# Performance work log

Measured on AMD Instinct MI355X. Metric: run time of the kernel, lower is better.

## Reference

```python
import jax, jax.numpy as jnp
import numpy as np

N, NOBJ, M, H, W = 512, 16, 8192, 128, 128


def _rand_rotations(key, n):
    A = jax.random.normal(key, (n, 3, 3), dtype=jnp.float32)
    q, r = jnp.linalg.qr(A)
    q = q * jnp.sign(jnp.diagonal(r, axis1=-2, axis2=-1))[:, None, :]
    det = jnp.linalg.det(q)  # +-1; flip first column if det == -1
    q = q.at[:, :, 0].multiply(det[:, None])
    return q


def setup_inputs() -> dict:
    key = jax.random.key(0)
    ks = jax.random.split(key, 10)
    obj_id = jax.random.randint(ks[0], (N,), 0, NOBJ, dtype=jnp.int32)
    # realistic pinhole intrinsics (pixels), slight per-sample jitter
    base_K = jnp.array([[600.0, 0.0, 64.0], [0.0, 600.0, 64.0], [0.0, 0.0, 1.0]], jnp.float32)
    cam_K = base_K[None] + jax.random.normal(ks[1], (N, 3, 3)) * jnp.array(
        [[5.0, 0.0, 1.0], [0.0, 5.0, 1.0], [0.0, 0.0, 0.0]], jnp.float32)
    gt_R = _rand_rotations(ks[2], N)
    # small rotational perturbation for pred
    pred_R = _rand_rotations(ks[3], N) @ gt_R
    gt_t = jnp.concatenate([jax.random.normal(ks[4], (N, 2)) * 20.0,
                            500.0 + jax.random.uniform(ks[4], (N, 1)) * 300.0], axis=-1)
    pred_t = gt_t + jax.random.normal(ks[5], (N, 3)) * 5.0
    mesh_points = jax.random.normal(ks[6], (NOBJ, M, 3)) * 50.0  # mm-scale meshes
    diameters = 150.0 + jax.random.uniform(ks[7], (NOBJ,)) * 150.0
    gt_coord_3d_roi = jax.random.normal(ks[8], (N, 3, H, W)) * 50.0
    gt_mask_vis_roi = jax.random.bernoulli(ks[9], 0.4, (N, 1, H, W))
    return dict(obj_id=obj_id, cam_K=cam_K, gt_cam_R_m2c=gt_R, gt_cam_t_m2c=gt_t,
                pred_cam_R_m2c=pred_R, pred_cam_t_m2c=pred_t,
                gt_coord_3d_roi=gt_coord_3d_roi, gt_mask_vis_roi=gt_mask_vis_roi,
                mesh_points=mesh_points, diameters=diameters)


def _project(K, x):
    # K: [N,3,3], x: [N,...,3] -> pixel coords [N,...,2]
    h = jnp.einsum('nij,n...j->n...i', K, x)
    return h[..., :2] / h[..., 2:3]


def reference(obj_id, cam_K, gt_cam_R_m2c, gt_cam_t_m2c, pred_cam_R_m2c,
              pred_cam_t_m2c, gt_coord_3d_roi, gt_mask_vis_roi, mesh_points, diameters):
    # RE (degrees)
    R_diff = pred_cam_R_m2c @ jnp.swapaxes(gt_cam_R_m2c, -2, -1)
    trace = R_diff[..., 0, 0] + R_diff[..., 1, 1] + R_diff[..., 2, 2]
    re = jnp.arccos((jnp.clip(trace, -1.0, 3.0) - 1.0) * 0.5) * (180.0 / jnp.pi)
    # TE (cm)
    te = jnp.linalg.norm(pred_cam_t_m2c - gt_cam_t_m2c, axis=-1) * 100.0
    # ADD: mean distance between transformed mesh points, / diameter
    pts = mesh_points[obj_id]                      # [N,M,3]
    dR = pred_cam_R_m2c - gt_cam_R_m2c
    dt = pred_cam_t_m2c - gt_cam_t_m2c
    diff = jnp.einsum('nij,nmj->nmi', dR, pts) + dt[:, None, :]
    ad = jnp.linalg.norm(diff, axis=-1).mean(axis=-1) / diameters[obj_id]
    # PROJ: mean projected distance over mesh points
    xp = jnp.einsum('nij,nmj->nmi', pred_cam_R_m2c, pts) + pred_cam_t_m2c[:, None, :]
    xg = jnp.einsum('nij,nmj->nmi', gt_cam_R_m2c, pts) + gt_cam_t_m2c[:, None, :]
    pj = jnp.linalg.norm(_project(cam_K, xp) - _project(cam_K, xg), axis=-1).mean(axis=-1)
    # PROJ-visible: same over visible ROI pixels (masked mean instead of ragged gather)
    verts = jnp.transpose(gt_coord_3d_roi, (0, 2, 3, 1))  # [N,H,W,3]
    vp = jnp.einsum('nij,nhwj->nhwi', pred_cam_R_m2c, verts) + pred_cam_t_m2c[:, None, None, :]
    vg = jnp.einsum('nij,nhwj->nhwi', gt_cam_R_m2c, verts) + gt_cam_t_m2c[:, None, None, :]
    d = jnp.linalg.norm(_project(cam_K, vp) - _project(cam_K, vg), axis=-1)  # [N,H,W]
    mask = gt_mask_vis_roi[:, 0].astype(d.dtype)
    pv = (d * mask).sum(axis=(1, 2)) / jnp.maximum(mask.sum(axis=(1, 2)), 1.0)
    return re, te, ad, pj, pv
```

## Files before the change

kernel.cpp:

```cpp
#include <hip/hip_runtime.h>
#include <math.h>

#define NS    512
#define NOBJ  16
#define MPTS  8192
#define HH    128
#define WW    128
#define HW    (HH * WW)
#define BLOCK 256
#define SPLIT 4
#define NWAVE (BLOCK / 64)
#define P_IT  (HW / 4 / SPLIT / BLOCK)
#define M_IT  (MPTS / SPLIT / (BLOCK * 4))

__device__ __forceinline__ float frcp(float x)  { return __builtin_amdgcn_rcpf(x); }
__device__ __forceinline__ float fsqrt(float x) { return __builtin_amdgcn_sqrtf(x); }
__device__ __forceinline__ float rfl(float x) {
    return __int_as_float(__builtin_amdgcn_readfirstlane(__float_as_int(x)));
}
__device__ __forceinline__ void sched_fence() {
#if __has_builtin(__builtin_amdgcn_sched_barrier)
    __builtin_amdgcn_sched_barrier(0);
#endif
}

__device__ __forceinline__ void fuse_proj(const float* __restrict__ cam_K,
                                          const float* __restrict__ R,
                                          const float* __restrict__ t, int n,
                                          float A[9], float b[3]) {
    float K[9], Rr[9], tt[3];
#pragma unroll
    for (int i = 0; i < 9; ++i) { K[i] = cam_K[n * 9 + i]; Rr[i] = R[n * 9 + i]; }
#pragma unroll
    for (int i = 0; i < 3; ++i) tt[i] = t[n * 3 + i];
#pragma unroll
    for (int r = 0; r < 3; ++r) {
#pragma unroll
        for (int c = 0; c < 3; ++c)
            A[r * 3 + c] = rfl(K[r * 3 + 0] * Rr[0 * 3 + c]
                             + K[r * 3 + 1] * Rr[1 * 3 + c]
                             + K[r * 3 + 2] * Rr[2 * 3 + c]);
        b[r] = rfl(K[r * 3 + 0] * tt[0] + K[r * 3 + 1] * tt[1] + K[r * 3 + 2] * tt[2]);
    }
}

__global__ __attribute__((amdgpu_flat_work_group_size(BLOCK, BLOCK),
                          amdgpu_waves_per_eu(3, 4)))
void score_partial(
    const int*   __restrict__ obj_id,
    const float* __restrict__ cam_K,
    const float* __restrict__ gt_R,
    const float* __restrict__ gt_t,
    const float* __restrict__ pr_R,
    const float* __restrict__ pr_t,
    const float* __restrict__ coord,
    const int*   __restrict__ mask,
    const float* __restrict__ mesh,
    float*       __restrict__ ws)
{
    const int b   = blockIdx.x;
    const int n   = b >> 2;
    const int c   = b & (SPLIT - 1);
    const int tid = threadIdx.x;

    float Ap[9], Ag[9], bp[3], bg[3], dR[9], dt[3];
    fuse_proj(cam_K, pr_R, pr_t, n, Ap, bp);
    fuse_proj(cam_K, gt_R, gt_t, n, Ag, bg);
#pragma unroll
    for (int i = 0; i < 9; ++i) dR[i] = rfl(pr_R[n * 9 + i] - gt_R[n * 9 + i]);
#pragma unroll
    for (int i = 0; i < 3; ++i) dt[i] = rfl(pr_t[n * 3 + i] - gt_t[n * 3 + i]);
    const int obj = __builtin_amdgcn_readfirstlane(obj_id[n]);

    const float* cx = coord + (size_t)n * 3 * HW;
    const float4* cx4 = (const float4*)cx;
    const float4* cy4 = (const float4*)(cx + HW);
    const float4* cz4 = (const float4*)(cx + 2 * HW);
    const int4*   mk4 = (const int4*)(mask + (size_t)n * HW);
    const float4* mp4 = (const float4*)(mesh + (size_t)obj * MPTS * 3);

    float4 AX[P_IT], AY[P_IT], AZ[P_IT];
    int4   AM[P_IT];
#pragma unroll
    for (int it = 0; it < P_IT; ++it) {
        const int p = c * (HW / 4 / SPLIT) + it * BLOCK + tid;
        AX[it] = cx4[p];
        AY[it] = cy4[p];
        AZ[it] = cz4[p];
        AM[it] = mk4[p];
    }
    float4 MF[M_IT][3];
#pragma unroll
    for (int it = 0; it < M_IT; ++it) {
        const int k = c * (MPTS / SPLIT / 4) + it * BLOCK + tid;
        MF[it][0] = mp4[k * 3 + 0];
        MF[it][1] = mp4[k * 3 + 1];
        MF[it][2] = mp4[k * 3 + 2];
    }

    sched_fence();

    float s_pv = 0.0f, s_m = 0.0f;
#pragma unroll
    for (int it = 0; it < P_IT; ++it) {
        const float xs[4] = {AX[it].x, AX[it].y, AX[it].z, AX[it].w};
        const float ys[4] = {AY[it].x, AY[it].y, AY[it].z, AY[it].w};
        const float zs[4] = {AZ[it].x, AZ[it].y, AZ[it].z, AZ[it].w};
        const int   ms[4] = {AM[it].x, AM[it].y, AM[it].z, AM[it].w};
#pragma unroll
        for (int j = 0; j < 4; ++j) {
            const float x = xs[j], y = ys[j], z = zs[j];
            const float hpx = fmaf(Ap[0], x, fmaf(Ap[1], y, fmaf(Ap[2], z, bp[0])));
            const float hpy = fmaf(Ap[3], x, fmaf(Ap[4], y, fmaf(Ap[5], z, bp[1])));
            const float hpz = fmaf(Ap[6], x, fmaf(Ap[7], y, fmaf(Ap[8], z, bp[2])));
            const float hgx = fmaf(Ag[0], x, fmaf(Ag[1], y, fmaf(Ag[2], z, bg[0])));
            const float hgy = fmaf(Ag[3], x, fmaf(Ag[4], y, fmaf(Ag[5], z, bg[1])));
            const float hgz = fmaf(Ag[6], x, fmaf(Ag[7], y, fmaf(Ag[8], z, bg[2])));
            const float iwp = frcp(hpz), iwg = frcp(hgz);
            const float du = fmaf(hpx, iwp, -hgx * iwg);
            const float dv = fmaf(hpy, iwp, -hgy * iwg);
            const float d  = fsqrt(fmaf(du, du, dv * dv));
            const float fm = (ms[j] != 0) ? 1.0f : 0.0f;
            s_pv += d * fm;
            s_m  += fm;
        }
    }

    float s_ad = 0.0f, s_pj = 0.0f;
#pragma unroll
    for (int it = 0; it < M_IT; ++it) {
        const float4 f0 = MF[it][0], f1 = MF[it][1], f2 = MF[it][2];
        const float px[4] = {f0.x, f0.w, f1.z, f2.y};
        const float py[4] = {f0.y, f1.x, f1.w, f2.z};
        const float pz[4] = {f0.z, f1.y, f2.x, f2.w};
#pragma unroll
        for (int j = 0; j < 4; ++j) {
            const float x = px[j], y = py[j], z = pz[j];
            const float dx = fmaf(dR[0], x, fmaf(dR[1], y, fmaf(dR[2], z, dt[0])));
            const float dy = fmaf(dR[3], x, fmaf(dR[4], y, fmaf(dR[5], z, dt[1])));
            const float dz = fmaf(dR[6], x, fmaf(dR[7], y, fmaf(dR[8], z, dt[2])));
            s_ad += fsqrt(fmaf(dx, dx, fmaf(dy, dy, dz * dz)));
            const float hpx = fmaf(Ap[0], x, fmaf(Ap[1], y, fmaf(Ap[2], z, bp[0])));
            const float hpy = fmaf(Ap[3], x, fmaf(Ap[4], y, fmaf(Ap[5], z, bp[1])));
            const float hpz = fmaf(Ap[6], x, fmaf(Ap[7], y, fmaf(Ap[8], z, bp[2])));
            const float hgx = fmaf(Ag[0], x, fmaf(Ag[1], y, fmaf(Ag[2], z, bg[0])));
            const float hgy = fmaf(Ag[3], x, fmaf(Ag[4], y, fmaf(Ag[5], z, bg[1])));
            const float hgz = fmaf(Ag[6], x, fmaf(Ag[7], y, fmaf(Ag[8], z, bg[2])));
            const float iwp = frcp(hpz), iwg = frcp(hgz);
            const float du = fmaf(hpx, iwp, -hgx * iwg);
            const float dv = fmaf(hpy, iwp, -hgy * iwg);
            s_pj += fsqrt(fmaf(du, du, dv * dv));
        }
    }

    float vals[4] = {s_ad, s_pj, s_pv, s_m};
#pragma unroll
    for (int k = 0; k < 4; ++k)
#pragma unroll
        for (int off = 32; off > 0; off >>= 1)
            vals[k] += __shfl_down(vals[k], off, 64);

    __shared__ float red[4][NWAVE];
    const int wave = tid >> 6, lane = tid & 63;
    if (lane == 0) {
#pragma unroll
        for (int k = 0; k < 4; ++k) red[k][wave] = vals[k];
    }
    __syncthreads();
    if (tid == 0) {
#pragma unroll
        for (int k = 0; k < 4; ++k) {
            float s = 0.0f;
#pragma unroll
            for (int w = 0; w < NWAVE; ++w) s += red[k][w];
            ws[(size_t)(n * SPLIT + c) * 4 + k] = s;
        }
    }
}

__global__ __launch_bounds__(256) void score_reduce(
    const float* __restrict__ ws,
    const int*   __restrict__ obj_id,
    const float* __restrict__ gt_R,
    const float* __restrict__ gt_t,
    const float* __restrict__ pr_R,
    const float* __restrict__ pr_t,
    const float* __restrict__ diam,
    float*       __restrict__ out)
{
    const int n = blockIdx.x * blockDim.x + threadIdx.x;
    if (n >= NS) return;

    float ad = 0.0f, pj = 0.0f, pv = 0.0f, m = 0.0f;
#pragma unroll
    for (int cb = 0; cb < SPLIT; ++cb) {
        const float* p = ws + (size_t)(n * SPLIT + cb) * 4;
        ad += p[0]; pj += p[1]; pv += p[2]; m += p[3];
    }

    float trace = 0.0f;
#pragma unroll
    for (int i = 0; i < 9; ++i) trace += pr_R[n * 9 + i] * gt_R[n * 9 + i];
    trace = fminf(fmaxf(trace, -1.0f), 3.0f);
    const float dx = pr_t[n * 3 + 0] - gt_t[n * 3 + 0];
    const float dy = pr_t[n * 3 + 1] - gt_t[n * 3 + 1];
    const float dz = pr_t[n * 3 + 2] - gt_t[n * 3 + 2];

    const float dia = diam[obj_id[n]];
    out[0 * NS + n] = acosf((trace - 1.0f) * 0.5f) * (180.0f / 3.14159265358979323846f);
    out[1 * NS + n] = sqrtf(dx * dx + dy * dy + dz * dz) * 100.0f;
    out[2 * NS + n] = ad * (1.0f / MPTS) / dia;
    out[3 * NS + n] = pj * (1.0f / MPTS);
    out[4 * NS + n] = pv / fmaxf(m, 1.0f);
}

extern "C" void kernel_launch(void* const* d_in, const int* in_sizes, int n_in,
                              void* d_out, int out_size, void* d_ws, size_t ws_size,
                              hipStream_t stream) {
    const int*   obj_id = (const int*)  d_in[0];
    const float* cam_K  = (const float*)d_in[1];
    const float* gt_R   = (const float*)d_in[2];
    const float* gt_t   = (const float*)d_in[3];
    const float* pr_R   = (const float*)d_in[4];
    const float* pr_t   = (const float*)d_in[5];
    const float* coord  = (const float*)d_in[6];
    const int*   mask   = (const int*)  d_in[7];
    const float* mesh   = (const float*)d_in[8];
    const float* diam   = (const float*)d_in[9];
    float* out = (float*)d_out;
    float* ws  = (float*)d_ws;

    score_partial<<<NS * SPLIT, BLOCK, 0, stream>>>(obj_id, cam_K, gt_R, gt_t, pr_R,
                                                    pr_t, coord, mask, mesh, ws);
    score_reduce<<<(NS + 255) / 256, 256, 0, stream>>>(ws, obj_id, gt_R, gt_t,
                                                       pr_R, pr_t, diam, out);
}
```

Baseline: 192.0 us.

## Fuse partial and reduce kernels into one block-per-sample kernel with prefetch pipeline

Replaces the two-kernel scheme (4 blocks per sample writing partials, then a reduce kernel) with one 512-thread block per sample that writes final outputs directly. ROI data is streamed through a 4-slot register ring with 3-deep software prefetch and nontemporal loads, instead of loading everything up front. Mesh loads are moved after the ROI loop. This removes a launch and the workspace round-trip, at the cost of fewer blocks (512) to fill the GPU and a serialised per-block pipeline.

```diff
diff --git a/kernel.cpp b/kernel.cpp
--- a/kernel.cpp
+++ b/kernel.cpp
@@ -7,11 +7,13 @@
 #define HH    128
 #define WW    128
 #define HW    (HH * WW)
-#define BLOCK 256
-#define SPLIT 4
+#define BLOCK 512
 #define NWAVE (BLOCK / 64)
-#define P_IT  (HW / 4 / SPLIT / BLOCK)
-#define M_IT  (MPTS / SPLIT / (BLOCK * 4))
+#define P_IT  (HW / 4 / BLOCK)
+#define M_IT  (MPTS / 4 / BLOCK)
+
+typedef float f4 __attribute__((ext_vector_type(4)));
+typedef int   i4 __attribute__((ext_vector_type(4)));
 
 __device__ __forceinline__ float frcp(float x)  { return __builtin_amdgcn_rcpf(x); }
 __device__ __forceinline__ float fsqrt(float x) { return __builtin_amdgcn_sqrtf(x); }
@@ -21,6 +23,20 @@
 __device__ __forceinline__ void sched_fence() {
 #if __has_builtin(__builtin_amdgcn_sched_barrier)
     __builtin_amdgcn_sched_barrier(0);
+#endif
+}
+__device__ __forceinline__ f4 ntl_f4(const f4* p) {
+#if __has_builtin(__builtin_nontemporal_load)
+    return __builtin_nontemporal_load(p);
+#else
+    return *p;
+#endif
+}
+__device__ __forceinline__ i4 ntl_i4(const i4* p) {
+#if __has_builtin(__builtin_nontemporal_load)
+    return __builtin_nontemporal_load(p);
+#else
+    return *p;
 #endif
 }
 
@@ -45,8 +61,8 @@
 }
 
 __global__ __attribute__((amdgpu_flat_work_group_size(BLOCK, BLOCK),
-                          amdgpu_waves_per_eu(3, 4)))
-void score_partial(
+                          amdgpu_waves_per_eu(4, 4)))
+void score_kernel(
     const int*   __restrict__ obj_id,
     const float* __restrict__ cam_K,
     const float* __restrict__ gt_R,
@@ -56,11 +72,10 @@
     const float* __restrict__ coord,
     const int*   __restrict__ mask,
     const float* __restrict__ mesh,
-    float*       __restrict__ ws)
+    const float* __restrict__ diam,
+    float*       __restrict__ out)
 {
-    const int b   = blockIdx.x;
-    const int n   = b >> 2;
-    const int c   = b & (SPLIT - 1);
+    const int n   = blockIdx.x;
     const int tid = threadIdx.x;
 
     float Ap[9], Ag[9], bp[3], bg[3], dR[9], dt[3];
@@ -73,40 +88,40 @@
     const int obj = __builtin_amdgcn_readfirstlane(obj_id[n]);
 
     const float* cx = coord + (size_t)n * 3 * HW;
-    const float4* cx4 = (const float4*)cx;
-    const float4* cy4 = (const float4*)(cx + HW);
-    const float4* cz4 = (const float4*)(cx + 2 * HW);
-    const int4*   mk4 = (const int4*)(mask + (size_t)n * HW);
-    const float4* mp4 = (const float4*)(mesh + (size_t)obj * MPTS * 3);
-
-    float4 AX[P_IT], AY[P_IT], AZ[P_IT];
-    int4   AM[P_IT];
+    const f4* cx4 = (const f4*)cx;
+    const f4* cy4 = (const f4*)(cx + HW);
+    const f4* cz4 = (const f4*)(cx + 2 * HW);
+    const i4* mk4 = (const i4*)(mask + (size_t)n * HW);
+
+    f4 AX[4], AY[4], AZ[4];
+    i4 AM[4];
+#pragma unroll
+    for (int t = 0; t < 3; ++t) {
+        const int p = t * BLOCK + tid;
+        AX[t] = ntl_f4(cx4 + p);
+        AY[t] = ntl_f4(cy4 + p);
+        AZ[t] = ntl_f4(cz4 + p);
+        AM[t] = ntl_i4(mk4 + p);
+    }
+
+    float s_pv = 0.0f, s_m = 0.0f;
 #pragma unroll
     for (int it = 0; it < P_IT; ++it) {
-        const int p = c * (HW / 4 / SPLIT) + it * BLOCK + tid;
-        AX[it] = cx4[p];
-        AY[it] = cy4[p];
-        AZ[it] = cz4[p];
-        AM[it] = mk4[p];
-    }
-    float4 MF[M_IT][3];
-#pragma unroll
-    for (int it = 0; it < M_IT; ++it) {
-        const int k = c * (MPTS / SPLIT / 4) + it * BLOCK + tid;
-        MF[it][0] = mp4[k * 3 + 0];
-        MF[it][1] = mp4[k * 3 + 1];
-        MF[it][2] = mp4[k * 3 + 2];
-    }
-
-    sched_fence();
-
-    float s_pv = 0.0f, s_m = 0.0f;
-#pragma unroll
-    for (int it = 0; it < P_IT; ++it) {
-        const float xs[4] = {AX[it].x, AX[it].y, AX[it].z, AX[it].w};
-        const float ys[4] = {AY[it].x, AY[it].y, AY[it].z, AY[it].w};
-        const float zs[4] = {AZ[it].x, AZ[it].y, AZ[it].z, AZ[it].w};
-        const int   ms[4] = {AM[it].x, AM[it].y, AM[it].z, AM[it].w};
+        if (it + 3 < P_IT) {
+            const int t = it + 3;
+            const int s = t & 3;
+            const int p = t * BLOCK + tid;
+            AX[s] = ntl_f4(cx4 + p);
+            AY[s] = ntl_f4(cy4 + p);
+            AZ[s] = ntl_f4(cz4 + p);
+            AM[s] = ntl_i4(mk4 + p);
+        }
+        sched_fence();
+        const int s = it & 3;
+        const float xs[4] = {AX[s].x, AX[s].y, AX[s].z, AX[s].w};
+        const float ys[4] = {AY[s].x, AY[s].y, AY[s].z, AY[s].w};
+        const float zs[4] = {AZ[s].x, AZ[s].y, AZ[s].z, AZ[s].w};
+        const int   ms[4] = {AM[s].x, AM[s].y, AM[s].z, AM[s].w};
 #pragma unroll
         for (int j = 0; j < 4; ++j) {
             const float x = xs[j], y = ys[j], z = zs[j];
@@ -126,10 +141,21 @@
         }
     }
 
+    const f4* mp4 = (const f4*)(mesh + (size_t)obj * MPTS * 3);
+    f4 MF[M_IT][3];
+#pragma unroll
+    for (int it = 0; it < M_IT; ++it) {
+        const int k = it * BLOCK + tid;
+        MF[it][0] = mp4[k * 3 + 0];
+        MF[it][1] = mp4[k * 3 + 1];
+        MF[it][2] = mp4[k * 3 + 2];
+    }
+    sched_fence();
+
     float s_ad = 0.0f, s_pj = 0.0f;
 #pragma unroll
     for (int it = 0; it < M_IT; ++it) {
-        const float4 f0 = MF[it][0], f1 = MF[it][1], f2 = MF[it][2];
+        const f4 f0 = MF[it][0], f1 = MF[it][1], f2 = MF[it][2];
         const float px[4] = {f0.x, f0.w, f1.z, f2.y};
         const float py[4] = {f0.y, f1.x, f1.w, f2.z};
         const float pz[4] = {f0.z, f1.y, f2.x, f2.w};
@@ -167,51 +193,31 @@
         for (int k = 0; k < 4; ++k) red[k][wave] = vals[k];
     }
     __syncthreads();
+
     if (tid == 0) {
+        float tot[4];
 #pragma unroll
         for (int k = 0; k < 4; ++k) {
             float s = 0.0f;
 #pragma unroll
             for (int w = 0; w < NWAVE; ++w) s += red[k][w];
-            ws[(size_t)(n * SPLIT + c) * 4 + k] = s;
-        }
-    }
-}
-
-__global__ __launch_bounds__(256) void score_reduce(
-    const float* __restrict__ ws,
-    const int*   __restrict__ obj_id,
-    const float* __restrict__ gt_R,
-    const float* __restrict__ gt_t,
-    const float* __restrict__ pr_R,
-    const float* __restrict__ pr_t,
-    const float* __restrict__ diam,
-    float*       __restrict__ out)
-{
-    const int n = blockIdx.x * blockDim.x + threadIdx.x;
-    if (n >= NS) return;
-
-    float ad = 0.0f, pj = 0.0f, pv = 0.0f, m = 0.0f;
-#pragma unroll
-    for (int cb = 0; cb < SPLIT; ++cb) {
-        const float* p = ws + (size_t)(n * SPLIT + cb) * 4;
-        ad += p[0]; pj += p[1]; pv += p[2]; m += p[3];
-    }
-
-    float trace = 0.0f;
-#pragma unroll
-    for (int i = 0; i < 9; ++i) trace += pr_R[n * 9 + i] * gt_R[n * 9 + i];
-    trace = fminf(fmaxf(trace, -1.0f), 3.0f);
-    const float dx = pr_t[n * 3 + 0] - gt_t[n * 3 + 0];
-    const float dy = pr_t[n * 3 + 1] - gt_t[n * 3 + 1];
-    const float dz = pr_t[n * 3 + 2] - gt_t[n * 3 + 2];
-
-    const float dia = diam[obj_id[n]];
-    out[0 * NS + n] = acosf((trace - 1.0f) * 0.5f) * (180.0f / 3.14159265358979323846f);
-    out[1 * NS + n] = sqrtf(dx * dx + dy * dy + dz * dz) * 100.0f;
-    out[2 * NS + n] = ad * (1.0f / MPTS) / dia;
-    out[3 * NS + n] = pj * (1.0f / MPTS);
-    out[4 * NS + n] = pv / fmaxf(m, 1.0f);
+            tot[k] = s;
+        }
+        float Rg9[9], Rp9[9];
+#pragma unroll
+        for (int i = 0; i < 9; ++i) { Rg9[i] = gt_R[n * 9 + i]; Rp9[i] = pr_R[n * 9 + i]; }
+        float trace = 0.0f;
+#pragma unroll
+        for (int i = 0; i < 9; ++i) trace += Rp9[i] * Rg9[i];
+        trace = fminf(fmaxf(trace, -1.0f), 3.0f);
+        const float te = sqrtf(dt[0] * dt[0] + dt[1] * dt[1] + dt[2] * dt[2]) * 100.0f;
+
+        out[0 * NS + n] = acosf((trace - 1.0f) * 0.5f) * (180.0f / 3.14159265358979323846f);
+        out[1 * NS + n] = te;
+        out[2 * NS + n] = tot[0] * (1.0f / MPTS) / diam[obj];
+        out[3 * NS + n] = tot[1] * (1.0f / MPTS);
+        out[4 * NS + n] = tot[2] / fmaxf(tot[3], 1.0f);
+    }
 }
 
 extern "C" void kernel_launch(void* const* d_in, const int* in_sizes, int n_in,
@@ -228,10 +234,7 @@
     const float* mesh   = (const float*)d_in[8];
     const float* diam   = (const float*)d_in[9];
     float* out = (float*)d_out;
-    float* ws  = (float*)d_ws;
-
-    score_partial<<<NS * SPLIT, BLOCK, 0, stream>>>(obj_id, cam_K, gt_R, gt_t, pr_R,
-                                                    pr_t, coord, mask, mesh, ws);
-    score_reduce<<<(NS + 255) / 256, 256, 0, stream>>>(ws, obj_id, gt_R, gt_t,
-                                                       pr_R, pr_t, diam, out);
-}
+
+    score_kernel<<<NS, BLOCK, 0, stream>>>(obj_id, cam_K, gt_R, gt_t, pr_R, pr_t,
+                                           coord, mask, mesh, diam, out);
+}
```

After: 184.4 us. 4.0% less time.

## Stage ROI pixel tiles into LDS via async global_load_lds with staged waits

Applied to the files above, without the earlier changes.

Replaces the per-thread register prefetch of coord and mask float4s with direct global-to-LDS DMA (global_load_lds), issued as four tiles per block. Each tile's compute starts after a partial vmcnt wait, so later tiles keep loading while earlier ones are processed. The aim is to cut VGPR pressure and overlap memory with compute. In exchange each block now holds a 64 KB LDS buffer, which caps blocks per CU. The waves_per_eu hint is also removed, so occupancy may drop.

```diff
diff --git a/kernel.cpp b/kernel.cpp
--- a/kernel.cpp
+++ b/kernel.cpp
@@ -1,17 +1,26 @@
 #include <hip/hip_runtime.h>
 #include <math.h>
 
-#define NS    512
-#define NOBJ  16
-#define MPTS  8192
-#define HH    128
-#define WW    128
-#define HW    (HH * WW)
-#define BLOCK 256
-#define SPLIT 4
-#define NWAVE (BLOCK / 64)
-#define P_IT  (HW / 4 / SPLIT / BLOCK)
-#define M_IT  (MPTS / SPLIT / (BLOCK * 4))
+#define NS     512
+#define NOBJ   16
+#define MPTS   8192
+#define HH     128
+#define WW     128
+#define HW     (HH * WW)
+#define BLOCK  256
+#define NWAVE  (BLOCK / 64)
+#define SPLIT  4
+#define CHUNK  (HW / SPLIT)
+#define TILE   1024
+#define NTILE  (CHUNK / TILE)
+#define SEG    (TILE / NWAVE)
+#define M_IT   (MPTS / SPLIT / (BLOCK * 4))
+
+typedef float f4 __attribute__((ext_vector_type(4)));
+typedef int   i4 __attribute__((ext_vector_type(4)));
+
+typedef const void __attribute__((address_space(1)))* gas1_t;
+typedef void       __attribute__((address_space(3)))* las3_t;
 
 __device__ __forceinline__ float frcp(float x)  { return __builtin_amdgcn_rcpf(x); }
 __device__ __forceinline__ float fsqrt(float x) { return __builtin_amdgcn_sqrtf(x); }
@@ -22,6 +31,11 @@
 #if __has_builtin(__builtin_amdgcn_sched_barrier)
     __builtin_amdgcn_sched_barrier(0);
 #endif
+}
+#define WAIT_VM(n) __builtin_amdgcn_s_waitcnt((n) | (7 << 4) | (0xF << 8))
+
+__device__ __forceinline__ void dma16(const void* g, void* l) {
+    __builtin_amdgcn_global_load_lds((gas1_t)g, (las3_t)l, 16, 0, 0);
 }
 
 __device__ __forceinline__ void fuse_proj(const float* __restrict__ cam_K,
@@ -44,9 +58,50 @@
     }
 }
 
-__global__ __attribute__((amdgpu_flat_work_group_size(BLOCK, BLOCK),
-                          amdgpu_waves_per_eu(3, 4)))
-void score_partial(
+__device__ __forceinline__ void stage_tile(const float* cx, const float* cy,
+                                           const float* cz, const int* mk,
+                                           float* lds, int slot, int gofs, int wofs) {
+    float* base = lds + slot * (4 * TILE) + wofs;
+    dma16(cx + gofs, base + 0 * TILE);
+    dma16(cy + gofs, base + 1 * TILE);
+    dma16(cz + gofs, base + 2 * TILE);
+    dma16((const float*)mk + gofs, base + 3 * TILE);
+}
+
+__device__ __forceinline__ void compute_tile(const float* lds, int slot, int wofs,
+                                             int lane, const float Ap[9],
+                                             const float Ag[9], const float bp[3],
+                                             const float bg[3],
+                                             float& s_pv, float& s_m) {
+    const float* base = lds + slot * (4 * TILE) + wofs + 4 * lane;
+    const f4 vx = *(const f4*)(base + 0 * TILE);
+    const f4 vy = *(const f4*)(base + 1 * TILE);
+    const f4 vz = *(const f4*)(base + 2 * TILE);
+    const i4 mm = *(const i4*)(base + 3 * TILE);
+    const float xs[4] = {vx.x, vx.y, vx.z, vx.w};
+    const float ys[4] = {vy.x, vy.y, vy.z, vy.w};
+    const float zs[4] = {vz.x, vz.y, vz.z, vz.w};
+    const int   ms[4] = {mm.x, mm.y, mm.z, mm.w};
+#pragma unroll
+    for (int j = 0; j < 4; ++j) {
+        const float x = xs[j], y = ys[j], z = zs[j];
+        const float hpx = fmaf(Ap[0], x, fmaf(Ap[1], y, fmaf(Ap[2], z, bp[0])));
+        const float hpy = fmaf(Ap[3], x, fmaf(Ap[4], y, fmaf(Ap[5], z, bp[1])));
+        const float hpz = fmaf(Ap[6], x, fmaf(Ap[7], y, fmaf(Ap[8], z, bp[2])));
+        const float hgx = fmaf(Ag[0], x, fmaf(Ag[1], y, fmaf(Ag[2], z, bg[0])));
+        const float hgy = fmaf(Ag[3], x, fmaf(Ag[4], y, fmaf(Ag[5], z, bg[1])));
+        const float hgz = fmaf(Ag[6], x, fmaf(Ag[7], y, fmaf(Ag[8], z, bg[2])));
+        const float iwp = frcp(hpz), iwg = frcp(hgz);
+        const float du = fmaf(hpx, iwp, -hgx * iwg);
+        const float dv = fmaf(hpy, iwp, -hgy * iwg);
+        const float d  = fsqrt(fmaf(du, du, dv * dv));
+        const float fm = (ms[j] != 0) ? 1.0f : 0.0f;
+        s_pv += d * fm;
+        s_m  += fm;
+    }
+}
+
+__global__ __launch_bounds__(BLOCK) void score_partial(
     const int*   __restrict__ obj_id,
     const float* __restrict__ cam_K,
     const float* __restrict__ gt_R,
@@ -58,10 +113,16 @@
     const float* __restrict__ mesh,
     float*       __restrict__ ws)
 {
-    const int b   = blockIdx.x;
-    const int n   = b >> 2;
-    const int c   = b & (SPLIT - 1);
-    const int tid = threadIdx.x;
+    __shared__ float lds[4 * 4 * TILE];
+    __shared__ float red[4][NWAVE];
+
+    const int b    = blockIdx.x;
+    const int n    = b >> 2;
+    const int c    = b & (SPLIT - 1);
+    const int tid  = threadIdx.x;
+    const int w    = tid >> 6;
+    const int lane = tid & 63;
+    const int wofs = w * SEG;
 
     float Ap[9], Ag[9], bp[3], bg[3], dR[9], dt[3];
     fuse_proj(cam_K, pr_R, pr_t, n, Ap, bp);
@@ -73,23 +134,19 @@
     const int obj = __builtin_amdgcn_readfirstlane(obj_id[n]);
 
     const float* cx = coord + (size_t)n * 3 * HW;
-    const float4* cx4 = (const float4*)cx;
-    const float4* cy4 = (const float4*)(cx + HW);
-    const float4* cz4 = (const float4*)(cx + 2 * HW);
-    const int4*   mk4 = (const int4*)(mask + (size_t)n * HW);
-    const float4* mp4 = (const float4*)(mesh + (size_t)obj * MPTS * 3);
-
-    float4 AX[P_IT], AY[P_IT], AZ[P_IT];
-    int4   AM[P_IT];
-#pragma unroll
-    for (int it = 0; it < P_IT; ++it) {
-        const int p = c * (HW / 4 / SPLIT) + it * BLOCK + tid;
-        AX[it] = cx4[p];
-        AY[it] = cy4[p];
-        AZ[it] = cz4[p];
-        AM[it] = mk4[p];
-    }
-    float4 MF[M_IT][3];
+    const float* cy = cx + HW;
+    const float* cz = cx + 2 * HW;
+    const int*   mk = mask + (size_t)n * HW;
+    const int chunkBase = c * CHUNK;
+    const int laneofs   = wofs + 4 * lane;
+
+    stage_tile(cx, cy, cz, mk, lds, 0, chunkBase + 0 * TILE + laneofs, wofs);
+    stage_tile(cx, cy, cz, mk, lds, 1, chunkBase + 1 * TILE + laneofs, wofs);
+    stage_tile(cx, cy, cz, mk, lds, 2, chunkBase + 2 * TILE + laneofs, wofs);
+    stage_tile(cx, cy, cz, mk, lds, 3, chunkBase + 3 * TILE + laneofs, wofs);
+
+    const f4* mp4 = (const f4*)(mesh + (size_t)obj * MPTS * 3);
+    f4 MF[M_IT][3];
 #pragma unroll
     for (int it = 0; it < M_IT; ++it) {
         const int k = c * (MPTS / SPLIT / 4) + it * BLOCK + tid;
@@ -97,39 +154,22 @@
         MF[it][1] = mp4[k * 3 + 1];
         MF[it][2] = mp4[k * 3 + 2];
     }
-
     sched_fence();
 
     float s_pv = 0.0f, s_m = 0.0f;
-#pragma unroll
-    for (int it = 0; it < P_IT; ++it) {
-        const float xs[4] = {AX[it].x, AX[it].y, AX[it].z, AX[it].w};
-        const float ys[4] = {AY[it].x, AY[it].y, AY[it].z, AY[it].w};
-        const float zs[4] = {AZ[it].x, AZ[it].y, AZ[it].z, AZ[it].w};
-        const int   ms[4] = {AM[it].x, AM[it].y, AM[it].z, AM[it].w};
-#pragma unroll
-        for (int j = 0; j < 4; ++j) {
-            const float x = xs[j], y = ys[j], z = zs[j];
-            const float hpx = fmaf(Ap[0], x, fmaf(Ap[1], y, fmaf(Ap[2], z, bp[0])));
-            const float hpy = fmaf(Ap[3], x, fmaf(Ap[4], y, fmaf(Ap[5], z, bp[1])));
-            const float hpz = fmaf(Ap[6], x, fmaf(Ap[7], y, fmaf(Ap[8], z, bp[2])));
-            const float hgx = fmaf(Ag[0], x, fmaf(Ag[1], y, fmaf(Ag[2], z, bg[0])));
-            const float hgy = fmaf(Ag[3], x, fmaf(Ag[4], y, fmaf(Ag[5], z, bg[1])));
-            const float hgz = fmaf(Ag[6], x, fmaf(Ag[7], y, fmaf(Ag[8], z, bg[2])));
-            const float iwp = frcp(hpz), iwg = frcp(hgz);
-            const float du = fmaf(hpx, iwp, -hgx * iwg);
-            const float dv = fmaf(hpy, iwp, -hgy * iwg);
-            const float d  = fsqrt(fmaf(du, du, dv * dv));
-            const float fm = (ms[j] != 0) ? 1.0f : 0.0f;
-            s_pv += d * fm;
-            s_m  += fm;
-        }
-    }
+    WAIT_VM(12); sched_fence();
+    compute_tile(lds, 0, wofs, lane, Ap, Ag, bp, bg, s_pv, s_m);
+    WAIT_VM(8);  sched_fence();
+    compute_tile(lds, 1, wofs, lane, Ap, Ag, bp, bg, s_pv, s_m);
+    WAIT_VM(4);  sched_fence();
+    compute_tile(lds, 2, wofs, lane, Ap, Ag, bp, bg, s_pv, s_m);
+    WAIT_VM(0);  sched_fence();
+    compute_tile(lds, 3, wofs, lane, Ap, Ag, bp, bg, s_pv, s_m);
 
     float s_ad = 0.0f, s_pj = 0.0f;
 #pragma unroll
     for (int it = 0; it < M_IT; ++it) {
-        const float4 f0 = MF[it][0], f1 = MF[it][1], f2 = MF[it][2];
+        const f4 f0 = MF[it][0], f1 = MF[it][1], f2 = MF[it][2];
         const float px[4] = {f0.x, f0.w, f1.z, f2.y};
         const float py[4] = {f0.y, f1.x, f1.w, f2.z};
         const float pz[4] = {f0.z, f1.y, f2.x, f2.w};
@@ -160,11 +200,9 @@
         for (int off = 32; off > 0; off >>= 1)
             vals[k] += __shfl_down(vals[k], off, 64);
 
-    __shared__ float red[4][NWAVE];
-    const int wave = tid >> 6, lane = tid & 63;
     if (lane == 0) {
 #pragma unroll
-        for (int k = 0; k < 4; ++k) red[k][wave] = vals[k];
+        for (int k = 0; k < 4; ++k) red[k][w] = vals[k];
     }
     __syncthreads();
     if (tid == 0) {
@@ -172,7 +210,7 @@
         for (int k = 0; k < 4; ++k) {
             float s = 0.0f;
 #pragma unroll
-            for (int w = 0; w < NWAVE; ++w) s += red[k][w];
+            for (int wv = 0; wv < NWAVE; ++wv) s += red[k][wv];
             ws[(size_t)(n * SPLIT + c) * 4 + k] = s;
         }
     }
```

Result: no change. 193.7 us (+0.9%).
